# Optimization experiments

Measured on AMD Instinct MI355X. Metric: run time of the kernel, lower is better.

## Reference

```python
import jax, jax.numpy as jnp
import numpy as np
import math

B, N, D, H = 2, 2048, 512, 8
DH = D // H
HID = int(D * 16 / 3)  # 2730, SwiGLU hidden; chunks into 1365+1365
EPS = 1e-5


def _get_slopes(n):
    # n=8 is a power of two
    start = 2.0 ** (-2.0 ** (-(math.log2(n) - 3)))
    return np.array([start * (start ** i) for i in range(n)], dtype=np.float32)

_SLOPES = jnp.asarray(_get_slopes(H))  # [H]


def _ln(x, w, b):
    m = jnp.mean(x, axis=-1, keepdims=True)
    v = jnp.mean((x - m) ** 2, axis=-1, keepdims=True)
    return (x - m) * jax.lax.rsqrt(v + EPS) * w + b


def setup_inputs() -> dict:
    key = jax.random.key(0)
    ks = jax.random.split(key, 20)
    p = lambda k, s: jax.random.normal(k, s, jnp.float32) * 0.02
    return {
        "x": jax.random.normal(ks[0], (B, N, D), jnp.float32),
        "coords": jax.random.uniform(ks[1], (B, N, 2), jnp.float32) * 100.0,
        "q_w": p(ks[2], (D, D)), "q_b": jnp.zeros((D,), jnp.float32),
        "k_w": p(ks[3], (D, D)), "k_b": jnp.zeros((D,), jnp.float32),
        "v_w": p(ks[4], (D, D)), "v_b": jnp.zeros((D,), jnp.float32),
        "o_w": p(ks[5], (D, D)), "o_b": jnp.zeros((D,), jnp.float32),
        "gamma1": jnp.ones((D,), jnp.float32),
        "ln1_w": jnp.ones((D,), jnp.float32), "ln1_b": jnp.zeros((D,), jnp.float32),
        "fc1_w": p(ks[6], (HID, D)), "fc1_b": jnp.zeros((HID,), jnp.float32),
        "fc2_w": p(ks[7], (D, HID // 2)), "fc2_b": jnp.zeros((D,), jnp.float32),
        "gamma2": jnp.ones((D,), jnp.float32),
        "ln2_w": jnp.ones((D,), jnp.float32), "ln2_b": jnp.zeros((D,), jnp.float32),
    }


def reference(x, coords, q_w, q_b, k_w, k_b, v_w, v_b, o_w, o_b, gamma1,
              ln1_w, ln1_b, fc1_w, fc1_b, fc2_w, fc2_b, gamma2, ln2_w, ln2_b):
    # ---- residual1: distance-ALiBi attention (eval mode: x + gamma1*attn(norm(x)))
    xn = _ln(x, ln1_w, ln1_b)
    q = (xn @ q_w.T + q_b).reshape(B, N, H, DH).transpose(0, 2, 1, 3)  # [b,h,n,dh]
    k = (xn @ k_w.T + k_b).reshape(B, N, H, DH).transpose(0, 2, 1, 3)
    v = (xn @ v_w.T + v_b).reshape(B, N, H, DH).transpose(0, 2, 1, 3)
    # pairwise Euclidean distance of tile coords -> [b,n,n]
    diff = coords[:, :, None, :] - coords[:, None, :, :]
    dist = jnp.sqrt(jnp.sum(diff * diff, axis=-1))
    attn_bias = -_SLOPES[None, :, None, None] * dist[:, None, :, :]  # [b,h,n,n]
    scale = 1.0 / math.sqrt(DH)
    scores = jnp.einsum('bhqd,bhkd->bhqk', q, k) * scale + attn_bias
    attn = jax.nn.softmax(scores, axis=-1)
    ctx = jnp.einsum('bhqk,bhkd->bhqd', attn, v)
    ctx = ctx.transpose(0, 2, 1, 3).reshape(B, N, D)
    attn_out = ctx @ o_w.T + o_b
    x = x + gamma1 * attn_out
    # ---- residual2: SwiGLU-style MLP (eval mode: x + gamma2*mlp(norm(x)))
    xn2 = _ln(x, ln2_w, ln2_b)
    hpre = xn2 @ fc1_w.T + fc1_b  # [b,n,HID]
    h1, h2 = jnp.split(hpre, 2, axis=-1)
    mlp_out = (jax.nn.silu(h1) * h2) @ fc2_w.T + fc2_b
    return x + gamma2 * mlp_out
```

## Files before the change

kernel.cpp:

```cpp
#include <hip/hip_runtime.h>
#include <math.h>

#define Bdim  2
#define Nseq  2048
#define Dmod  512
#define Hn    8
#define DHd   64
#define HID   2730
#define HHALF 1365
#define HC    1408
#define NPACK 2816
#define ROWS  4096

typedef __bf16 bf16x8 __attribute__((ext_vector_type(8)));
typedef __bf16 bf16x4 __attribute__((ext_vector_type(4)));
typedef float  f32x4  __attribute__((ext_vector_type(4)));

__device__ __forceinline__ void glds16(const __bf16* g, __bf16* l) {
    __builtin_amdgcn_global_load_lds(
        (const __attribute__((address_space(1))) void*)g,
        (__attribute__((address_space(3))) void*)l, 16, 0, 0);
}

#define SEG0 (1536*512)
#define SEG1 (512*512)
#define SEG2 (NPACK*512)
#define SEG3 (512*HC)
__global__ __launch_bounds__(256) void convert_all(
    const float* __restrict__ q_w, const float* __restrict__ k_w,
    const float* __restrict__ v_w, const float* __restrict__ o_w,
    const float* __restrict__ fc1_w, const float* __restrict__ fc2_w,
    __bf16* __restrict__ wqkv, __bf16* __restrict__ wo,
    __bf16* __restrict__ wfc1p, __bf16* __restrict__ wfc2p)
{
    int idx = blockIdx.x * 256 + threadIdx.x;
    if (idx < SEG0) {
        int n = idx >> 9, k = idx & 511;
        float v = (n < 512) ? q_w[n * 512 + k]
                : (n < 1024) ? k_w[(n - 512) * 512 + k]
                : v_w[(n - 1024) * 512 + k];
        wqkv[idx] = (__bf16)v;
        return;
    }
    idx -= SEG0;
    if (idx < SEG1) { wo[idx] = (__bf16)o_w[idx]; return; }
    idx -= SEG1;
    if (idx < SEG2) {
        int n = idx >> 9, k = idx & 511;
        int j = n >> 5, u = n & 31;
        int base = j * 16 + (u & 15);
        float v = 0.0f;
        if (base < HHALF) {
            int hidx = base + ((u & 16) ? HHALF : 0);
            v = fc1_w[(size_t)hidx * 512 + k];
        }
        wfc1p[idx] = (__bf16)v;
        return;
    }
    idx -= SEG2;
    if (idx < SEG3) {
        int n = idx / HC, k = idx - n * HC;
        float v = (k < HHALF) ? fc2_w[(size_t)n * HHALF + k] : 0.0f;
        wfc2p[idx] = (__bf16)v;
    }
}

__global__ __launch_bounds__(256) void ln_kernel(
    const float* __restrict__ x, const float* __restrict__ w,
    const float* __restrict__ b, __bf16* __restrict__ out)
{
    const int row = blockIdx.x;
    const int tid = threadIdx.x;
    const float* xr = x + (size_t)row * Dmod;
    float2 v = *(const float2*)(xr + tid * 2);
    float s  = v.x + v.y;
    float sq = v.x * v.x + v.y * v.y;
#pragma unroll
    for (int m = 1; m < 64; m <<= 1) {
        s  += __shfl_xor(s, m, 64);
        sq += __shfl_xor(sq, m, 64);
    }
    __shared__ float ss[4], ssq[4];
    const int wv = tid >> 6;
    if ((tid & 63) == 0) { ss[wv] = s; ssq[wv] = sq; }
    __syncthreads();
    s  = ss[0] + ss[1] + ss[2] + ss[3];
    sq = ssq[0] + ssq[1] + ssq[2] + ssq[3];
    const float mean = s * (1.0f / Dmod);
    const float var  = sq * (1.0f / Dmod) - mean * mean;
    const float rstd = rsqrtf(var + 1e-5f);
    float2 wv2 = *(const float2*)(w + tid * 2);
    float2 bv2 = *(const float2*)(b + tid * 2);
    __bf16* orow = out + (size_t)row * Dmod + tid * 2;
    orow[0] = (__bf16)((v.x - mean) * rstd * wv2.x + bv2.x);
    orow[1] = (__bf16)((v.y - mean) * rstd * wv2.y + bv2.y);
}

__global__ __launch_bounds__(256) void gemm_res(
    const __bf16* __restrict__ A, int lda,
    const __bf16* __restrict__ Bw, int ldb,
    const float* __restrict__ bias, int K,
    float* __restrict__ out_f32, int ld_out,
    const float* __restrict__ res, const float* __restrict__ g)
{
    __shared__ __bf16 As[64][40];
    __shared__ __bf16 Bs[64][40];
    const int tid  = threadIdx.x;
    const int wave = tid >> 6, lane = tid & 63;
    const int t    = lane & 15, quad = lane >> 4;
    const int m0   = blockIdx.x * 64;
    const int n0   = blockIdx.y * 64;
    const int sr   = tid >> 2, sc = (tid & 3) * 8;

    f32x4 acc[4] = {};
    bf16x8 av = *(const bf16x8*)(A  + (size_t)(m0 + sr) * lda + sc);
    bf16x8 bv = *(const bf16x8*)(Bw + (size_t)(n0 + sr) * ldb + sc);

    for (int k0 = 0; k0 < K; k0 += 32) {
        __syncthreads();
        *(bf16x8*)(&As[sr][sc]) = av;
        *(bf16x8*)(&Bs[sr][sc]) = bv;
        __syncthreads();
        if (k0 + 32 < K) {
            av = *(const bf16x8*)(A  + (size_t)(m0 + sr) * lda + (k0 + 32 + sc));
            bv = *(const bf16x8*)(Bw + (size_t)(n0 + sr) * ldb + (k0 + 32 + sc));
        }
        bf16x8 a = *(const bf16x8*)(&As[wave * 16 + t][quad * 8]);
#pragma unroll
        for (int ct = 0; ct < 4; ++ct) {
            bf16x8 b = *(const bf16x8*)(&Bs[ct * 16 + t][quad * 8]);
            acc[ct] = __builtin_amdgcn_mfma_f32_16x16x32_bf16(a, b, acc[ct], 0, 0, 0);
        }
    }

    const int row_base = m0 + wave * 16 + quad * 4;
#pragma unroll
    for (int ct = 0; ct < 4; ++ct) {
        const int col = n0 + ct * 16 + t;
        const float bb = bias[col];
#pragma unroll
        for (int r = 0; r < 4; ++r) {
            const int row = row_base + r;
            out_f32[(size_t)row * ld_out + col] =
                res[(size_t)row * ld_out + col] + g[col] * (acc[ct][r] + bb);
        }
    }
}

__global__ __launch_bounds__(256) void qkv_gemm128(
    const __bf16* __restrict__ A, const __bf16* __restrict__ W,
    const float* __restrict__ qb_, const float* __restrict__ kb_,
    const float* __restrict__ vb_,
    __bf16* __restrict__ qk, __bf16* __restrict__ vtg)
{
    __shared__ __bf16 As[128 * 32];
    __shared__ __bf16 Bs[128 * 32];
    const int tid  = threadIdx.x;
    const int wave = tid >> 6, lane = tid & 63;
    const int t    = lane & 15, quad = lane >> 4;
    const int m0   = blockIdx.x * 128, n0 = blockIdx.y * 128;
    const int mr   = (wave & 1) * 64,  nr = (wave >> 1) * 64;
    const int ra0 = tid >> 2,          ca0 = (tid & 3) * 8;
    const int ra1 = (tid + 256) >> 2,  ca1 = (tid & 3) * 8;

    f32x4 acc[4][4] = {};

    for (int k0 = 0; k0 < Dmod; k0 += 32) {
        __syncthreads();
        glds16(A + (size_t)(m0 + ra0) * Dmod + k0 + ca0, As + tid * 8);
        glds16(A + (size_t)(m0 + ra1) * Dmod + k0 + ca1, As + (tid + 256) * 8);
        glds16(W + (size_t)(n0 + ra0) * Dmod + k0 + ca0, Bs + tid * 8);
        glds16(W + (size_t)(n0 + ra1) * Dmod + k0 + ca1, Bs + (tid + 256) * 8);
        __syncthreads();
        bf16x8 af[4], bfr[4];
#pragma unroll
        for (int mi = 0; mi < 4; ++mi)
            af[mi] = *(const bf16x8*)(As + (mr + mi * 16 + t) * 32 + quad * 8);
#pragma unroll
        for (int ni = 0; ni < 4; ++ni)
            bfr[ni] = *(const bf16x8*)(Bs + (nr + ni * 16 + t) * 32 + quad * 8);
#pragma unroll
        for (int mi = 0; mi < 4; ++mi)
#pragma unroll
            for (int ni = 0; ni < 4; ++ni)
                acc[mi][ni] = __builtin_amdgcn_mfma_f32_16x16x32_bf16(af[mi], bfr[ni], acc[mi][ni], 0, 0, 0);
    }

#pragma unroll
    for (int mi = 0; mi < 4; ++mi) {
        const int row_base = m0 + mr + mi * 16 + quad * 4;
#pragma unroll
        for (int ni = 0; ni < 4; ++ni) {
            const int col = n0 + nr + ni * 16 + t;
            const float bb = (col < 512) ? qb_[col]
                            : (col < 1024) ? kb_[col - 512] : vb_[col - 1024];
            if (col < 1024) {
#pragma unroll
                for (int r = 0; r < 4; ++r)
                    qk[(size_t)(row_base + r) * 1024 + col] = (__bf16)(acc[mi][ni][r] + bb);
            } else {
                const int f = col - 1024, hh = f >> 6, dh = f & 63;
                const int bI = row_base >> 11, n = row_base & 2047;
                bf16x4 pk;
#pragma unroll
                for (int r = 0; r < 4; ++r) pk[r] = (__bf16)(acc[mi][ni][r] + bb);
                *(bf16x4*)(vtg + ((size_t)((bI * 8 + hh) * 64 + dh)) * Nseq + n) = pk;
            }
        }
    }
}

__global__ __launch_bounds__(256) void fc1_gemm128(
    const __bf16* __restrict__ A, const __bf16* __restrict__ W,
    const float* __restrict__ fc1_b_, __bf16* __restrict__ out)
{
    __shared__ __bf16 As[128 * 32];
    __shared__ __bf16 Bs[128 * 32];
    const int tid  = threadIdx.x;
    const int wave = tid >> 6, lane = tid & 63;
    const int t    = lane & 15, quad = lane >> 4;
    const int m0   = blockIdx.x * 128, n0 = blockIdx.y * 128;
    const int mr   = (wave & 1) * 64,  nr = (wave >> 1) * 64;
    const int ra0 = tid >> 2,          ca0 = (tid & 3) * 8;
    const int ra1 = (tid + 256) >> 2,  ca1 = (tid & 3) * 8;

    f32x4 acc[4][4] = {};

    for (int k0 = 0; k0 < Dmod; k0 += 32) {
        __syncthreads();
        glds16(A + (size_t)(m0 + ra0) * Dmod + k0 + ca0, As + tid * 8);
        glds16(A + (size_t)(m0 + ra1) * Dmod + k0 + ca1, As + (tid + 256) * 8);
        glds16(W + (size_t)(n0 + ra0) * Dmod + k0 + ca0, Bs + tid * 8);
        glds16(W + (size_t)(n0 + ra1) * Dmod + k0 + ca1, Bs + (tid + 256) * 8);
        __syncthreads();
        bf16x8 af[4], bfr[4];
#pragma unroll
        for (int mi = 0; mi < 4; ++mi)
            af[mi] = *(const bf16x8*)(As + (mr + mi * 16 + t) * 32 + quad * 8);
#pragma unroll
        for (int ni = 0; ni < 4; ++ni)
            bfr[ni] = *(const bf16x8*)(Bs + (nr + ni * 16 + t) * 32 + quad * 8);
#pragma unroll
        for (int mi = 0; mi < 4; ++mi)
#pragma unroll
            for (int ni = 0; ni < 4; ++ni)
                acc[mi][ni] = __builtin_amdgcn_mfma_f32_16x16x32_bf16(af[mi], bfr[ni], acc[mi][ni], 0, 0, 0);
    }

#pragma unroll
    for (int mi = 0; mi < 4; ++mi) {
        const int row_base = m0 + mr + mi * 16 + quad * 4;
#pragma unroll
        for (int gI = 0; gI < 2; ++gI) {
            const int base = n0 + nr + gI * 32;
            const int hb = (base >> 5) * 16 + t;
            const bool valid = hb < HHALF;
            const float b1 = valid ? fc1_b_[hb] : 0.0f;
            const float b2 = valid ? fc1_b_[HHALF + hb] : 0.0f;
#pragma unroll
            for (int r = 0; r < 4; ++r) {
                float a = acc[mi][2 * gI][r] + b1;
                float c = acc[mi][2 * gI + 1][r] + b2;
                float sw = a / (1.0f + __expf(-a)) * c;
                out[(size_t)(row_base + r) * HC + hb] = (__bf16)sw;
            }
        }
    }
}

__global__ __launch_bounds__(256) void attn_kernel(
    const __bf16* __restrict__ qk, const __bf16* __restrict__ vt,
    const float* __restrict__ coords, __bf16* __restrict__ ctx)
{
    constexpr int LD = 72;
    __shared__ __bf16 Ks[64][LD];
    __shared__ __bf16 Vt[64][LD];
    __shared__ __bf16 Ps[64][LD];
    __shared__ float2 kco[64];

    const int qt = blockIdx.x, h = blockIdx.y, b = blockIdx.z;
    const int bh = b * Hn + h;
    const int tid = threadIdx.x;
    const int wave = tid >> 6, lane = tid & 63;
    const int t = lane & 15, quad = lane >> 4;
    const float c1 = 0.125f * 1.44269504f;
    const float d1 = exp2f(-(float)(h + 1)) * 1.44269504f;

    const int qrow = qt * 64 + wave * 16 + t;
    const size_t qbase = (size_t)(b * Nseq + qrow) * 1024 + h * DHd;
    bf16x8 bq0 = *(const bf16x8*)(qk + qbase + quad * 8);
    bf16x8 bq1 = *(const bf16x8*)(qk + qbase + 32 + quad * 8);
    float2 qc = *(const float2*)(coords + (size_t)(b * Nseq + qrow) * 2);
    const float qx = qc.x, qy = qc.y;

    const int sr = tid >> 3, scc = (tid & 7) * 8;
    const __bf16* kbase = qk + (size_t)(b * Nseq) * 1024 + 512 + h * DHd;
    const __bf16* vbase = vt + (size_t)(bh * 64) * Nseq;

    bf16x8 kreg0, kreg1, vreg0, vreg1;
    float2 kcreg = {0.f, 0.f};
    kreg0 = *(const bf16x8*)(kbase + (size_t)sr * 1024 + scc);
    kreg1 = *(const bf16x8*)(kbase + (size_t)(sr + 32) * 1024 + scc);
    vreg0 = *(const bf16x8*)(vbase + (size_t)sr * Nseq + scc);
    vreg1 = *(const bf16x8*)(vbase + (size_t)(sr + 32) * Nseq + scc);
    if (tid < 64) kcreg = *(const float2*)(coords + (size_t)(b * Nseq + tid) * 2);

    f32x4 o[4] = {};
    float lrun = 0.0f;

    for (int kt = 0; kt < Nseq / 64; ++kt) {
        __syncthreads();
        *(bf16x8*)(&Ks[sr][scc])      = kreg0;
        *(bf16x8*)(&Ks[sr + 32][scc]) = kreg1;
        *(bf16x8*)(&Vt[sr][scc])      = vreg0;
        *(bf16x8*)(&Vt[sr + 32][scc]) = vreg1;
        if (tid < 64) kco[tid] = kcreg;
        __syncthreads();
        if (kt + 1 < Nseq / 64) {
            const int kn = (kt + 1) * 64;
            kreg0 = *(const bf16x8*)(kbase + (size_t)(kn + sr) * 1024 + scc);
            kreg1 = *(const bf16x8*)(kbase + (size_t)(kn + sr + 32) * 1024 + scc);
            vreg0 = *(const bf16x8*)(vbase + (size_t)sr * Nseq + kn + scc);
            vreg1 = *(const bf16x8*)(vbase + (size_t)(sr + 32) * Nseq + kn + scc);
            if (tid < 64) kcreg = *(const float2*)(coords + (size_t)(b * Nseq + kn + tid) * 2);
        }

        f32x4 s[4];
#pragma unroll
        for (int am = 0; am < 4; ++am) {
            bf16x8 a0 = *(const bf16x8*)(&Ks[am * 16 + t][quad * 8]);
            bf16x8 a1 = *(const bf16x8*)(&Ks[am * 16 + t][32 + quad * 8]);
            f32x4 z = {};
            z = __builtin_amdgcn_mfma_f32_16x16x32_bf16(a0, bq0, z, 0, 0, 0);
            s[am] = __builtin_amdgcn_mfma_f32_16x16x32_bf16(a1, bq1, z, 0, 0, 0);
        }

        float p[4][4];
#pragma unroll
        for (int am = 0; am < 4; ++am)
#pragma unroll
            for (int r = 0; r < 4; ++r) {
                float2 kc = kco[am * 16 + quad * 4 + r];
                float dx = qx - kc.x, dy = qy - kc.y;
                float e = exp2f(s[am][r] * c1 - d1 * sqrtf(dx * dx + dy * dy));
                p[am][r] = e;
                lrun += e;
            }

#pragma unroll
        for (int am = 0; am < 4; ++am) {
            bf16x4 pk;
#pragma unroll
            for (int r = 0; r < 4; ++r) pk[r] = (__bf16)p[am][r];
            *(bf16x4*)(&Ps[wave * 16 + t][am * 16 + quad * 4]) = pk;
        }

        bf16x8 ap0 = *(const bf16x8*)(&Ps[wave * 16 + t][quad * 8]);
        bf16x8 ap1 = *(const bf16x8*)(&Ps[wave * 16 + t][32 + quad * 8]);
#pragma unroll
        for (int ct = 0; ct < 4; ++ct) {
            bf16x8 bv0 = *(const bf16x8*)(&Vt[ct * 16 + t][quad * 8]);
            bf16x8 bv1 = *(const bf16x8*)(&Vt[ct * 16 + t][32 + quad * 8]);
            o[ct] = __builtin_amdgcn_mfma_f32_16x16x32_bf16(ap0, bv0, o[ct], 0, 0, 0);
            o[ct] = __builtin_amdgcn_mfma_f32_16x16x32_bf16(ap1, bv1, o[ct], 0, 0, 0);
        }
    }

    lrun += __shfl_xor(lrun, 16, 64);
    lrun += __shfl_xor(lrun, 32, 64);
    float rinv[4];
#pragma unroll
    for (int r = 0; r < 4; ++r) rinv[r] = 1.0f / __shfl(lrun, quad * 4 + r, 64);
    const int orow_base = qt * 64 + wave * 16 + quad * 4;
#pragma unroll
    for (int ct = 0; ct < 4; ++ct)
#pragma unroll
        for (int r = 0; r < 4; ++r) {
            size_t row = (size_t)b * Nseq + orow_base + r;
            ctx[row * Dmod + h * DHd + ct * 16 + t] = (__bf16)(o[ct][r] * rinv[r]);
        }
}

extern "C" void kernel_launch(void* const* d_in, const int* in_sizes, int n_in,
                              void* d_out, int out_size, void* d_ws, size_t ws_size,
                              hipStream_t stream)
{
    (void)in_sizes; (void)n_in; (void)out_size; (void)ws_size;
    const float* x      = (const float*)d_in[0];
    const float* coords = (const float*)d_in[1];
    const float* q_w    = (const float*)d_in[2];
    const float* q_b    = (const float*)d_in[3];
    const float* k_w    = (const float*)d_in[4];
    const float* k_b    = (const float*)d_in[5];
    const float* v_w    = (const float*)d_in[6];
    const float* v_b    = (const float*)d_in[7];
    const float* o_w    = (const float*)d_in[8];
    const float* o_b    = (const float*)d_in[9];
    const float* gamma1 = (const float*)d_in[10];
    const float* ln1_w  = (const float*)d_in[11];
    const float* ln1_b  = (const float*)d_in[12];
    const float* fc1_w  = (const float*)d_in[13];
    const float* fc1_b  = (const float*)d_in[14];
    const float* fc2_w  = (const float*)d_in[15];
    const float* fc2_b  = (const float*)d_in[16];
    const float* gamma2 = (const float*)d_in[17];
    const float* ln2_w  = (const float*)d_in[18];
    const float* ln2_b  = (const float*)d_in[19];

    size_t off = 0;
    auto alloc = [&](size_t bytes) {
        void* p = (char*)d_ws + off;
        off += (bytes + 255) & ~(size_t)255;
        return p;
    };
    __bf16* wqkv  = (__bf16*)alloc((size_t)1536 * 512 * 2);
    __bf16* wo    = (__bf16*)alloc((size_t)512 * 512 * 2);
    __bf16* wfc1p = (__bf16*)alloc((size_t)NPACK * 512 * 2);
    __bf16* wfc2p = (__bf16*)alloc((size_t)512 * HC * 2);
    __bf16* xn    = (__bf16*)alloc((size_t)ROWS * Dmod * 2);
    __bf16* xn2   = (__bf16*)alloc((size_t)ROWS * Dmod * 2);
    __bf16* qkb   = (__bf16*)alloc((size_t)ROWS * 1024 * 2);
    __bf16* vtg   = (__bf16*)alloc((size_t)Bdim * Hn * DHd * Nseq * 2);
    __bf16* ctxb  = (__bf16*)alloc((size_t)ROWS * Dmod * 2);
    float*  x1    = (float*)alloc((size_t)ROWS * Dmod * 4);
    __bf16* hcomb = (__bf16*)alloc((size_t)ROWS * HC * 2);

    const int conv_total = SEG0 + SEG1 + SEG2 + SEG3;
    convert_all<<<(conv_total + 255) / 256, 256, 0, stream>>>(
        q_w, k_w, v_w, o_w, fc1_w, fc2_w, wqkv, wo, wfc1p, wfc2p);

    ln_kernel<<<ROWS, 256, 0, stream>>>(x, ln1_w, ln1_b, xn);

    qkv_gemm128<<<dim3(ROWS / 128, 12), 256, 0, stream>>>(xn, wqkv, q_b, k_b, v_b, qkb, vtg);

    attn_kernel<<<dim3(Nseq / 64, Hn, Bdim), 256, 0, stream>>>(qkb, vtg, coords, ctxb);

    gemm_res<<<dim3(ROWS / 64, Dmod / 64), 256, 0, stream>>>(
        ctxb, Dmod, wo, Dmod, o_b, Dmod, x1, Dmod, x, gamma1);

    ln_kernel<<<ROWS, 256, 0, stream>>>(x1, ln2_w, ln2_b, xn2);

    fc1_gemm128<<<dim3(ROWS / 128, NPACK / 128), 256, 0, stream>>>(xn2, wfc1p, fc1_b, hcomb);

    gemm_res<<<dim3(ROWS / 64, Dmod / 64), 256, 0, stream>>>(
        hcomb, HC, wfc2p, HC, fc2_b, HC, (float*)d_out, Dmod, x1, gamma2);
}
```

Measured before the change: 261.5 us.

## Split attention over key dimension and merge partial sums in separate kernel

Splits the attention key loop into two halves across extra blocks (split-K), writing unnormalized fp32 partial outputs and row sums, then merges them in a new kernel that sums and normalizes to bf16. This doubles the attention grid from 512 to 1024 blocks so more of the GPU's compute units are busy. It also swaps sqrtf/exp2f for the raw AMDGCN intrinsics. The cost is extra fp32 traffic for the partials, plus one more kernel launch.

```diff
diff --git a/kernel.cpp b/kernel.cpp
--- a/kernel.cpp
+++ b/kernel.cpp
@@ -11,6 +11,8 @@
 #define HC    1408
 #define NPACK 2816
 #define ROWS  4096
+#define NSPLIT 2
+#define KT_PER (Nseq / 64 / NSPLIT)
 
 typedef __bf16 bf16x8 __attribute__((ext_vector_type(8)));
 typedef __bf16 bf16x4 __attribute__((ext_vector_type(4)));
@@ -270,7 +272,8 @@
 
 __global__ __launch_bounds__(256) void attn_kernel(
     const __bf16* __restrict__ qk, const __bf16* __restrict__ vt,
-    const float* __restrict__ coords, __bf16* __restrict__ ctx)
+    const float* __restrict__ coords,
+    float* __restrict__ op, float* __restrict__ lp)
 {
     constexpr int LD = 72;
     __shared__ __bf16 Ks[64][LD];
@@ -278,13 +281,15 @@
     __shared__ __bf16 Ps[64][LD];
     __shared__ float2 kco[64];
 
-    const int qt = blockIdx.x, h = blockIdx.y, b = blockIdx.z;
+    const int qt = blockIdx.x, h = blockIdx.y;
+    const int s = blockIdx.z >> 1, b = blockIdx.z & 1;
     const int bh = b * Hn + h;
     const int tid = threadIdx.x;
     const int wave = tid >> 6, lane = tid & 63;
     const int t = lane & 15, quad = lane >> 4;
     const float c1 = 0.125f * 1.44269504f;
     const float d1 = exp2f(-(float)(h + 1)) * 1.44269504f;
+    const int kt0 = s * KT_PER, kt1 = kt0 + KT_PER;
 
     const int qrow = qt * 64 + wave * 16 + t;
     const size_t qbase = (size_t)(b * Nseq + qrow) * 1024 + h * DHd;
@@ -299,16 +304,19 @@
 
     bf16x8 kreg0, kreg1, vreg0, vreg1;
     float2 kcreg = {0.f, 0.f};
-    kreg0 = *(const bf16x8*)(kbase + (size_t)sr * 1024 + scc);
-    kreg1 = *(const bf16x8*)(kbase + (size_t)(sr + 32) * 1024 + scc);
-    vreg0 = *(const bf16x8*)(vbase + (size_t)sr * Nseq + scc);
-    vreg1 = *(const bf16x8*)(vbase + (size_t)(sr + 32) * Nseq + scc);
-    if (tid < 64) kcreg = *(const float2*)(coords + (size_t)(b * Nseq + tid) * 2);
+    {
+        const int kn0 = kt0 * 64;
+        kreg0 = *(const bf16x8*)(kbase + (size_t)(kn0 + sr) * 1024 + scc);
+        kreg1 = *(const bf16x8*)(kbase + (size_t)(kn0 + sr + 32) * 1024 + scc);
+        vreg0 = *(const bf16x8*)(vbase + (size_t)sr * Nseq + kn0 + scc);
+        vreg1 = *(const bf16x8*)(vbase + (size_t)(sr + 32) * Nseq + kn0 + scc);
+        if (tid < 64) kcreg = *(const float2*)(coords + (size_t)(b * Nseq + kn0 + tid) * 2);
+    }
 
     f32x4 o[4] = {};
     float lrun = 0.0f;
 
-    for (int kt = 0; kt < Nseq / 64; ++kt) {
+    for (int kt = kt0; kt < kt1; ++kt) {
         __syncthreads();
         *(bf16x8*)(&Ks[sr][scc])      = kreg0;
         *(bf16x8*)(&Ks[sr + 32][scc]) = kreg1;
@@ -316,7 +324,7 @@
         *(bf16x8*)(&Vt[sr + 32][scc]) = vreg1;
         if (tid < 64) kco[tid] = kcreg;
         __syncthreads();
-        if (kt + 1 < Nseq / 64) {
+        if (kt + 1 < kt1) {
             const int kn = (kt + 1) * 64;
             kreg0 = *(const bf16x8*)(kbase + (size_t)(kn + sr) * 1024 + scc);
             kreg1 = *(const bf16x8*)(kbase + (size_t)(kn + sr + 32) * 1024 + scc);
@@ -325,14 +333,14 @@
             if (tid < 64) kcreg = *(const float2*)(coords + (size_t)(b * Nseq + kn + tid) * 2);
         }
 
-        f32x4 s[4];
+        f32x4 sA[4];
 #pragma unroll
         for (int am = 0; am < 4; ++am) {
             bf16x8 a0 = *(const bf16x8*)(&Ks[am * 16 + t][quad * 8]);
             bf16x8 a1 = *(const bf16x8*)(&Ks[am * 16 + t][32 + quad * 8]);
             f32x4 z = {};
             z = __builtin_amdgcn_mfma_f32_16x16x32_bf16(a0, bq0, z, 0, 0, 0);
-            s[am] = __builtin_amdgcn_mfma_f32_16x16x32_bf16(a1, bq1, z, 0, 0, 0);
+            sA[am] = __builtin_amdgcn_mfma_f32_16x16x32_bf16(a1, bq1, z, 0, 0, 0);
         }
 
         float p[4][4];
@@ -342,7 +350,8 @@
             for (int r = 0; r < 4; ++r) {
                 float2 kc = kco[am * 16 + quad * 4 + r];
                 float dx = qx - kc.x, dy = qy - kc.y;
-                float e = exp2f(s[am][r] * c1 - d1 * sqrtf(dx * dx + dy * dy));
+                float dist = __builtin_amdgcn_sqrtf(dx * dx + dy * dy);
+                float e = __builtin_amdgcn_exp2f(sA[am][r] * c1 - d1 * dist);
                 p[am][r] = e;
                 lrun += e;
             }
@@ -368,17 +377,38 @@
 
     lrun += __shfl_xor(lrun, 16, 64);
     lrun += __shfl_xor(lrun, 32, 64);
-    float rinv[4];
-#pragma unroll
-    for (int r = 0; r < 4; ++r) rinv[r] = 1.0f / __shfl(lrun, quad * 4 + r, 64);
+    if (quad == 0)
+        lp[(((size_t)s * Bdim + b) * Hn + h) * Nseq + qt * 64 + wave * 16 + t] = lrun;
+
     const int orow_base = qt * 64 + wave * 16 + quad * 4;
 #pragma unroll
     for (int ct = 0; ct < 4; ++ct)
 #pragma unroll
         for (int r = 0; r < 4; ++r) {
-            size_t row = (size_t)b * Nseq + orow_base + r;
-            ctx[row * Dmod + h * DHd + ct * 16 + t] = (__bf16)(o[ct][r] * rinv[r]);
-        }
+            size_t row = (size_t)s * ROWS + b * Nseq + orow_base + r;
+            op[row * Dmod + h * DHd + ct * 16 + t] = o[ct][r];
+        }
+}
+
+__global__ __launch_bounds__(256) void merge_kernel(
+    const float* __restrict__ op, const float* __restrict__ lp,
+    __bf16* __restrict__ ctx)
+{
+    int idx = blockIdx.x * 256 + threadIdx.x;
+    int row = idx >> 7, c4 = (idx & 127) * 4;
+    int h = c4 >> 6;
+    int b = row >> 11, n = row & 2047;
+    float l = lp[(((size_t)0 * Bdim + b) * Hn + h) * Nseq + n]
+            + lp[(((size_t)1 * Bdim + b) * Hn + h) * Nseq + n];
+    float rl = __builtin_amdgcn_rcpf(l);
+    float4 o0 = *(const float4*)(op + (size_t)row * Dmod + c4);
+    float4 o1 = *(const float4*)(op + ((size_t)ROWS + row) * Dmod + c4);
+    bf16x4 r;
+    r[0] = (__bf16)((o0.x + o1.x) * rl);
+    r[1] = (__bf16)((o0.y + o1.y) * rl);
+    r[2] = (__bf16)((o0.z + o1.z) * rl);
+    r[3] = (__bf16)((o0.w + o1.w) * rl);
+    *(bf16x4*)(ctx + (size_t)row * Dmod + c4) = r;
 }
 
 extern "C" void kernel_launch(void* const* d_in, const int* in_sizes, int n_in,
@@ -424,6 +454,8 @@
     __bf16* ctxb  = (__bf16*)alloc((size_t)ROWS * Dmod * 2);
     float*  x1    = (float*)alloc((size_t)ROWS * Dmod * 4);
     __bf16* hcomb = (__bf16*)alloc((size_t)ROWS * HC * 2);
+    float*  opb   = (float*)alloc((size_t)NSPLIT * ROWS * Dmod * 4);
+    float*  lpb   = (float*)alloc((size_t)NSPLIT * Bdim * Hn * Nseq * 4);
 
     const int conv_total = SEG0 + SEG1 + SEG2 + SEG3;
     convert_all<<<(conv_total + 255) / 256, 256, 0, stream>>>(
@@ -433,7 +465,9 @@
 
     qkv_gemm128<<<dim3(ROWS / 128, 12), 256, 0, stream>>>(xn, wqkv, q_b, k_b, v_b, qkb, vtg);
 
-    attn_kernel<<<dim3(Nseq / 64, Hn, Bdim), 256, 0, stream>>>(qkb, vtg, coords, ctxb);
+    attn_kernel<<<dim3(Nseq / 64, Hn, Bdim * NSPLIT), 256, 0, stream>>>(
+        qkb, vtg, coords, opb, lpb);
+    merge_kernel<<<(ROWS * 128 + 255) / 256, 256, 0, stream>>>(opb, lpb, ctxb);
 
     gemm_res<<<dim3(ROWS / 64, Dmod / 64), 256, 0, stream>>>(
         ctxb, Dmod, wo, Dmod, o_b, Dmod, x1, Dmod, x, gamma1);
```

Result: faster. 229.8 us (-12.1%).
